# Optimization experiments

Measured on AMD Instinct MI355X. Metric: run time of the kernel, lower is better.

## Reference

```python
import jax, jax.numpy as jnp
import numpy as np

N_NODES = 100000
N_EDGES = 1600000
N_GRAPHS = 256
K_HOPS = 3


def setup_inputs() -> dict:
    key = jax.random.key(0)
    ks = jax.random.split(key, 10)
    x = jax.random.normal(ks[0], (N_NODES, 32), dtype=jnp.float32)
    edge_index = jax.random.randint(ks[1], (2, N_EDGES), 0, N_NODES, dtype=jnp.int32)
    batch = jnp.sort(jax.random.randint(ks[2], (N_NODES,), 0, N_GRAPHS, dtype=jnp.int32))
    gcn_w = jax.random.normal(ks[3], (64, 32), dtype=jnp.float32) * 0.1
    gcn_b = jax.random.normal(ks[4], (64,), dtype=jnp.float32) * 0.1
    w1 = jax.random.normal(ks[5], (32, 64), dtype=jnp.float32) * 0.1
    b1 = jax.random.normal(ks[6], (32,), dtype=jnp.float32) * 0.1
    w2 = jax.random.normal(ks[7], (16, 32), dtype=jnp.float32) * 0.1
    b2 = jax.random.normal(ks[8], (16,), dtype=jnp.float32) * 0.1
    return {"x": x, "edge_index": edge_index, "batch": batch,
            "gcn_w": gcn_w, "gcn_b": gcn_b, "w1": w1, "b1": b1, "w2": w2, "b2": b2}


def reference(x, edge_index, batch, gcn_w, gcn_b, w1, b1, w2, b2):
    N = x.shape[0]
    src, dst = edge_index[0], edge_index[1]
    # GCN symmetric normalization with self-loops: deg = in-degree + 1
    deg = jax.ops.segment_sum(jnp.ones_like(src, dtype=x.dtype), dst, num_segments=N) + 1.0
    norm = deg ** -0.5  # [N]
    h = x
    for _ in range(K_HOPS):
        # edge message: norm[src] * h[src], scattered to dst, scaled by norm[dst];
        # self-loop contributes norm[i]^2 * h[i]
        msg = h[src] * norm[src][:, None]                     # [E, C]
        agg = jax.ops.segment_sum(msg, dst, num_segments=N)    # [N, C]
        h = norm[:, None] * agg + (norm * norm)[:, None] * h
    h = jax.nn.relu(h @ gcn_w.T + gcn_b)                       # [N, hidden]
    # global mean pool per graph
    counts = jax.ops.segment_sum(jnp.ones((N,), x.dtype), batch, num_segments=N_GRAPHS)
    sums = jax.ops.segment_sum(h, batch, num_segments=N_GRAPHS)
    h_avg = sums / jnp.maximum(counts, 1.0)[:, None]           # [G, hidden]
    # classifier (dropout = identity in eval)
    h1 = jax.nn.relu(h_avg @ w1.T + b1)
    logits = h1 @ w2.T + b2                                    # [G, nc]
    return logits
```

## Files before the change

### kernel.cpp

```cpp
#include <hip/hip_runtime.h>

constexpr int NW    = 391;
constexpr int CH    = 8192;
constexpr int CAP_B = 8192;
constexpr int CAP_C = 10240;

__device__ __forceinline__ unsigned bf16_rne(float x) {
    unsigned u = __float_as_uint(x);
    u += 0x7fffu + ((u >> 16) & 1u);
    return u >> 16;
}
__device__ __forceinline__ unsigned pack2(float even, float odd) {
    return bf16_rne(even) | (bf16_rne(odd) << 16);
}
__device__ __forceinline__ float lo_f(unsigned u) { return __uint_as_float(u << 16); }
__device__ __forceinline__ float hi_f(unsigned u) { return __uint_as_float(u & 0xffff0000u); }


__global__ __launch_bounds__(512) void k_bucket(const int* __restrict__ src,
                                                const int* __restrict__ dst, int E,
                                                int* __restrict__ wcur, int* __restrict__ packed) {
    __shared__ int h[256];
    __shared__ int base[256];
    int t = threadIdx.x;
    if (t < 256) h[t] = 0;
    __syncthreads();
    int b0 = blockIdx.x * CH;
    int cnt = min(CH, E - b0);
    if (cnt == CH) {
        const int4* d4 = (const int4*)(dst + b0);
        for (int i = t; i < CH / 4; i += 512) {
            int4 v = d4[i];
            atomicAdd(&h[v.x / NW], 1); atomicAdd(&h[v.y / NW], 1);
            atomicAdd(&h[v.z / NW], 1); atomicAdd(&h[v.w / NW], 1);
        }
    } else {
        for (int i = t; i < cnt; i += 512) atomicAdd(&h[dst[b0 + i] / NW], 1);
    }
    __syncthreads();
    if (t < 256) { base[t] = atomicAdd(&wcur[t], h[t]); h[t] = 0; }
    __syncthreads();
    if (cnt == CH) {
        const int4* d4 = (const int4*)(dst + b0);
        const int4* s4 = (const int4*)(src + b0);
        for (int i = t; i < CH / 4; i += 512) {
            int4 dv = d4[i];
            int4 sv = s4[i];
            int da[4] = {dv.x, dv.y, dv.z, dv.w};
            int sa[4] = {sv.x, sv.y, sv.z, sv.w};
#pragma unroll
            for (int j = 0; j < 4; ++j) {
                int w = da[j] / NW;
                int l = da[j] - w * NW;
                int r = atomicAdd(&h[w], 1);
                int pos = base[w] + r;
                if (pos < CAP_B) packed[w * CAP_B + pos] = (l << 17) | sa[j];
            }
        }
    } else {
        for (int i = t; i < cnt; i += 512) {
            int d = dst[b0 + i];
            int s = src[b0 + i];
            int w = d / NW;
            int l = d - w * NW;
            int r = atomicAdd(&h[w], 1);
            int pos = base[w] + r;
            if (pos < CAP_B) packed[w * CAP_B + pos] = (l << 17) | s;
        }
    }
}


__global__ __launch_bounds__(512) void k_window(const int* __restrict__ packed,
                                                const int* __restrict__ wcur,
                                                float* __restrict__ norm,
                                                int2* __restrict__ rng,
                                                int* __restrict__ csr, int N, int W) {
    __shared__ int hist[NW];
    __shared__ int scan[512];
    __shared__ int cur[NW];
    int t = threadIdx.x, w = blockIdx.x;
    int lo = w * NW, nwn = min(NW, N - lo);
    for (int i = t; i < NW; i += 512) hist[i] = 0;
    __syncthreads();
    int cnt = min(wcur[w], CAP_B);
    const int* pk = packed + (size_t)w * CAP_B;
    for (int e = t; e < cnt; e += 512) atomicAdd(&hist[pk[e] >> 17], 1);
    __syncthreads();
    int d = (t < nwn) ? hist[t] : 0;
    if (t < nwn) norm[lo + t] = rsqrtf((float)(d + 1));
    int pd = (t < nwn) ? ((d + 7) & ~7) : 0;
    scan[t] = pd;
    __syncthreads();
    for (int s = 1; s < 512; s <<= 1) {
        int add = (t >= s) ? scan[t - s] : 0;
        __syncthreads();
        scan[t] += add;
        __syncthreads();
    }
    int base = w * CAP_C;
    int cend = base + scan[t];
    if (t < nwn) {
        rng[lo + t] = make_int2(cend - pd, cend);
        cur[t] = cend - pd;
    }
    if (w == W - 1 && t == 0) { norm[N] = 1.f; rng[N] = make_int2(0, 0); }
    __syncthreads();
    for (int e = t; e < cnt; e += 512) {
        int p = pk[e];
        int pos = atomicAdd(&cur[p >> 17], 1);
        csr[pos] = p & 0x1FFFF;
    }
    __syncthreads();
    if (t < nwn) {
        for (int pos = cur[t]; pos < cend; ++pos) csr[pos] = N;
    }
}


__global__ void k_prep(const float4* __restrict__ x, const float* __restrict__ norm,
                       uint2* __restrict__ outb, int N) {
    int t = blockIdx.x * blockDim.x + threadIdx.x;
    int i = t >> 3;
    if (i < N) {
        float n = norm[i];
        float4 v = x[t];
        outb[t] = make_uint2(pack2(v.x * n, v.y * n), pack2(v.z * n, v.w * n));
    } else if (i == N) {
        outb[t] = make_uint2(0u, 0u);
    }
}

template <bool LAST>
__global__ void k_hop(const uint2* __restrict__ tab, const float* __restrict__ norm,
                      const int2* __restrict__ rng, const int* __restrict__ csr,
                      uint2* __restrict__ outb, int N) {
    int group = (blockIdx.x * blockDim.x + threadIdx.x) >> 3;
    int l = threadIdx.x & 7;
    if (group > N) return;
    uint2 sv = tab[(size_t)group * 8 + l];
    float ax = lo_f(sv.x), ay = hi_f(sv.x), az = lo_f(sv.y), aw = hi_f(sv.y);
    int2 be = rng[group];
    int k = be.x;
    for (; k + 16 <= be.y; k += 16) {
        int e0 = csr[k + l];
        int e1 = csr[k + 8 + l];
        uint2 u[16];
#pragma unroll
        for (int j = 0; j < 8; ++j) {
            int s = __shfl(e0, j, 8);
            u[j] = tab[(size_t)s * 8 + l];
        }
#pragma unroll
        for (int j = 0; j < 8; ++j) {
            int s = __shfl(e1, j, 8);
            u[8 + j] = tab[(size_t)s * 8 + l];
        }
#pragma unroll
        for (int j = 0; j < 16; ++j) {
            ax += lo_f(u[j].x); ay += hi_f(u[j].x);
            az += lo_f(u[j].y); aw += hi_f(u[j].y);
        }
    }
    if (k < be.y) {
        int e = csr[k + l];
        uint2 u[8];
#pragma unroll
        for (int j = 0; j < 8; ++j) {
            int s = __shfl(e, j, 8);
            u[j] = tab[(size_t)s * 8 + l];
        }
#pragma unroll
        for (int j = 0; j < 8; ++j) {
            ax += lo_f(u[j].x); ay += hi_f(u[j].x);
            az += lo_f(u[j].y); aw += hi_f(u[j].y);
        }
    }
    float n = norm[group];
    float sc = LAST ? n : n * n;
    outb[(size_t)group * 8 + l] = make_uint2(pack2(ax * sc, ay * sc), pack2(az * sc, aw * sc));
}


__global__ __launch_bounds__(256) void k_feat(const uint2* __restrict__ hb,
                                              const float* __restrict__ gw,
                                              const float* __restrict__ gb,
                                              uint4* __restrict__ zb4, int N) {
    __shared__ float w[64 * 32];
    __shared__ float bs[64];
    int t = threadIdx.x;
    for (int i = t; i < 64 * 32; i += 256) w[i] = gw[i];
    if (t < 64) bs[t] = gb[t];
    __syncthreads();
    int n = blockIdx.x * 256 + t;
    if (n >= N) return;
    float hrow[32];
    const uint2* hr = hb + (size_t)n * 8;
#pragma unroll
    for (int q = 0; q < 8; ++q) {
        uint2 u = hr[q];
        hrow[q * 4] = lo_f(u.x); hrow[q * 4 + 1] = hi_f(u.x);
        hrow[q * 4 + 2] = lo_f(u.y); hrow[q * 4 + 3] = hi_f(u.y);
    }
#pragma unroll
    for (int c0 = 0; c0 < 64; c0 += 16) {
        float o[16];
#pragma unroll
        for (int cc = 0; cc < 16; ++cc) {
            const float* wr = &w[(c0 + cc) * 32];
            float d = bs[c0 + cc];
#pragma unroll
            for (int k = 0; k < 32; ++k) d += hrow[k] * wr[k];
            o[cc] = fmaxf(d, 0.f);
        }
        zb4[(size_t)n * 8 + (c0 >> 3)] =
            make_uint4(pack2(o[0], o[1]), pack2(o[2], o[3]), pack2(o[4], o[5]), pack2(o[6], o[7]));
        zb4[(size_t)n * 8 + (c0 >> 3) + 1] =
            make_uint4(pack2(o[8], o[9]), pack2(o[10], o[11]), pack2(o[12], o[13]), pack2(o[14], o[15]));
    }
}


__global__ __launch_bounds__(256) void k_pool(const uint2* __restrict__ zb2,
                                              const int* __restrict__ batch, int N,
                                              const float* __restrict__ w1, const float* __restrict__ b1,
                                              const float* __restrict__ w2, const float* __restrict__ b2,
                                              float* __restrict__ out) {
    __shared__ float4 part[16][17];
    __shared__ float havg[64];
    __shared__ float h1s[32];
    __shared__ int se[2];
    int t = threadIdx.x, g = blockIdx.x;
    if (t < 2) {
        int target = g + t;
        int lo = 0, hi = N;
        while (lo < hi) { int mid = (lo + hi) >> 1; if (batch[mid] < target) lo = mid + 1; else hi = mid; }
        se[t] = lo;
    }
    __syncthreads();
    int start = se[0], end = se[1];
    int q = t & 15;
    int r = t >> 4;
    float4 acc = make_float4(0.f, 0.f, 0.f, 0.f);
    for (int n = start + r; n < end; n += 16) {
        uint2 v = zb2[(size_t)n * 16 + q];
        acc.x += lo_f(v.x); acc.y += hi_f(v.x); acc.z += lo_f(v.y); acc.w += hi_f(v.y);
    }
    part[r][q] = acc;
    __syncthreads();
#pragma unroll
    for (int s = 8; s > 0; s >>= 1) {
        if (r < s) {
            float4 a = part[r][q], b = part[r + s][q];
            a.x += b.x; a.y += b.y; a.z += b.z; a.w += b.w;
            part[r][q] = a;
        }
        __syncthreads();
    }
    if (t < 16) {
        int cnt = end - start;
        float inv = 1.f / (float)(cnt > 0 ? cnt : 1);
        float4 a = part[0][t];
        havg[t * 4] = a.x * inv; havg[t * 4 + 1] = a.y * inv;
        havg[t * 4 + 2] = a.z * inv; havg[t * 4 + 3] = a.w * inv;
    }
    __syncthreads();
    if (t < 32) {
        float d = b1[t];
#pragma unroll
        for (int k = 0; k < 64; ++k) d += havg[k] * w1[t * 64 + k];
        h1s[t] = fmaxf(d, 0.f);
    }
    __syncthreads();
    if (t < 16) {
        float d = b2[t];
#pragma unroll
        for (int j = 0; j < 32; ++j) d += h1s[j] * w2[t * 32 + j];
        out[g * 16 + t] = d;
    }
}


extern "C" void kernel_launch(void* const* d_in, const int* in_sizes, int n_in,
                              void* d_out, int out_size, void* d_ws, size_t ws_size,
                              hipStream_t stream) {
    const float* x     = (const float*)d_in[0];
    const int*   ei    = (const int*)d_in[1];
    const int*   batch = (const int*)d_in[2];
    const float* gw    = (const float*)d_in[3];
    const float* gb    = (const float*)d_in[4];
    const float* w1    = (const float*)d_in[5];
    const float* b1    = (const float*)d_in[6];
    const float* w2    = (const float*)d_in[7];
    const float* b2    = (const float*)d_in[8];
    float* out = (float*)d_out;

    int N = in_sizes[2];
    int E = in_sizes[1] / 2;
    int G = out_size / 16;
    const int* srcp = ei;
    const int* dstp = ei + E;

    int W  = (N + NW - 1) / NW;
    int NB = (E + CH - 1) / CH;

    char* ws = (char*)d_ws;
    size_t off = 0;
    auto alloc = [&](size_t bytes) -> void* {
        void* p = ws + off;
        off += (bytes + 255) & ~(size_t)255;
        return p;
    };
    int*   wcur   = (int*)alloc(256 * 4);
    int*   packed = (int*)alloc((size_t)W * CAP_B * 4);
    int*   csr    = (int*)alloc((size_t)W * CAP_C * 4);
    int2*  rng    = (int2*)alloc((size_t)(N + 1) * 8);
    float* norm   = (float*)alloc((size_t)(N + 1) * 4);
    uint2* hbA    = (uint2*)alloc((size_t)(N + 1) * 64);
    uint2* hbB    = (uint2*)alloc((size_t)(N + 1) * 64);
    unsigned* zbuf = (unsigned*)alloc((size_t)N * 64 * 2);

    hipMemsetAsync(wcur, 0, 256 * 4, stream);

    int pb = ((N + 1) * 8 + 255) / 256;

    k_bucket<<<NB, 512, 0, stream>>>(srcp, dstp, E, wcur, packed);
    k_window<<<W, 512, 0, stream>>>(packed, wcur, norm, rng, csr, N, W);

    k_prep<<<pb, 256, 0, stream>>>((const float4*)x, norm, hbA, N);
    k_hop<false><<<pb, 256, 0, stream>>>(hbA, norm, rng, csr, hbB, N);
    k_hop<false><<<pb, 256, 0, stream>>>(hbB, norm, rng, csr, hbA, N);
    k_hop<true ><<<pb, 256, 0, stream>>>(hbA, norm, rng, csr, hbB, N);

    k_feat<<<(N + 255) / 256, 256, 0, stream>>>(hbB, gw, gb, (uint4*)zbuf, N);
    k_pool<<<G, 256, 0, stream>>>((const uint2*)zbuf, batch, N, w1, b1, w2, b2, out);
}
```

Before: 203.8 us.

## Fuse prep into window kernel, widen hop gathers to 16B, use wave-shuffle scan

The bf16 feature-table prep (norm-scaled x) moves into k_window, which already holds the window's norms in shared memory, so one launch and one norm reread go away. The block prefix scan switches from a barrier-heavy shared-memory loop to wavefront shuffle scans. k_hop now has 4 lanes per node, each gathering a uint4 (8 bf16), and reads the CSR 8 edges at a time through int2 loads, dropping the 16-edge unrolled path. Each gather is wider and fewer threads are launched, but fewer independent loads are in flight per node, which may reduce memory-level parallelism.

```diff
diff --git a/kernel.cpp b/kernel.cpp
--- a/kernel.cpp
+++ b/kernel.cpp
@@ -73,12 +73,16 @@
 
 __global__ __launch_bounds__(512) void k_window(const int* __restrict__ packed,
                                                 const int* __restrict__ wcur,
+                                                const float4* __restrict__ x4,
                                                 float* __restrict__ norm,
                                                 int2* __restrict__ rng,
-                                                int* __restrict__ csr, int N, int W) {
+                                                int* __restrict__ csr,
+                                                uint2* __restrict__ hb, int N, int W) {
     __shared__ int hist[NW];
-    __shared__ int scan[512];
+    __shared__ float snorm[NW];
+    __shared__ int pend[NW];
     __shared__ int cur[NW];
+    __shared__ int wpart[8];
     int t = threadIdx.x, w = blockIdx.x;
     int lo = w * NW, nwn = min(NW, N - lo);
     for (int i = t; i < NW; i += 512) hist[i] = 0;
@@ -88,20 +92,34 @@
     for (int e = t; e < cnt; e += 512) atomicAdd(&hist[pk[e] >> 17], 1);
     __syncthreads();
     int d = (t < nwn) ? hist[t] : 0;
-    if (t < nwn) norm[lo + t] = rsqrtf((float)(d + 1));
+    float nv = rsqrtf((float)(d + 1));
+    if (t < nwn) { snorm[t] = nv; norm[lo + t] = nv; }
     int pd = (t < nwn) ? ((d + 7) & ~7) : 0;
-    scan[t] = pd;
-    __syncthreads();
-    for (int s = 1; s < 512; s <<= 1) {
-        int add = (t >= s) ? scan[t - s] : 0;
-        __syncthreads();
-        scan[t] += add;
-        __syncthreads();
-    }
+    int lane = t & 63, wid = t >> 6;
+    int v = pd;
+#pragma unroll
+    for (int s = 1; s < 64; s <<= 1) {
+        int u = __shfl_up(v, s, 64);
+        if (lane >= s) v += u;
+    }
+    if (lane == 63) wpart[wid] = v;
+    __syncthreads();
+    if (t < 8) {
+        int z = wpart[t];
+#pragma unroll
+        for (int s = 1; s < 8; s <<= 1) {
+            int u = __shfl_up(z, s, 8);
+            if (t >= s) z += u;
+        }
+        wpart[t] = z;
+    }
+    __syncthreads();
+    int incl = v + (wid ? wpart[wid - 1] : 0);
     int base = w * CAP_C;
-    int cend = base + scan[t];
+    int cend = base + incl;
     if (t < nwn) {
         rng[lo + t] = make_int2(cend - pd, cend);
+        pend[t] = cend;
         cur[t] = cend - pd;
     }
     if (w == W - 1 && t == 0) { norm[N] = 1.f; rng[N] = make_int2(0, 0); }
@@ -113,72 +131,50 @@
     }
     __syncthreads();
     if (t < nwn) {
-        for (int pos = cur[t]; pos < cend; ++pos) csr[pos] = N;
-    }
-}
-
-
-__global__ void k_prep(const float4* __restrict__ x, const float* __restrict__ norm,
-                       uint2* __restrict__ outb, int N) {
-    int t = blockIdx.x * blockDim.x + threadIdx.x;
-    int i = t >> 3;
-    if (i < N) {
-        float n = norm[i];
-        float4 v = x[t];
-        outb[t] = make_uint2(pack2(v.x * n, v.y * n), pack2(v.z * n, v.w * n));
-    } else if (i == N) {
-        outb[t] = make_uint2(0u, 0u);
-    }
+        for (int pos = cur[t]; pos < pend[t]; ++pos) csr[pos] = N;
+    }
+    for (int idx = t; idx < nwn * 8; idx += 512) {
+        int node = idx >> 3, q = idx & 7;
+        float nn = snorm[node];
+        float4 vx = x4[(size_t)(lo + node) * 8 + q];
+        hb[(size_t)(lo + node) * 8 + q] =
+            make_uint2(pack2(vx.x * nn, vx.y * nn), pack2(vx.z * nn, vx.w * nn));
+    }
+    if (w == W - 1 && t < 8) hb[(size_t)N * 8 + t] = make_uint2(0u, 0u);
 }
 
 template <bool LAST>
-__global__ void k_hop(const uint2* __restrict__ tab, const float* __restrict__ norm,
-                      const int2* __restrict__ rng, const int* __restrict__ csr,
-                      uint2* __restrict__ outb, int N) {
-    int group = (blockIdx.x * blockDim.x + threadIdx.x) >> 3;
-    int l = threadIdx.x & 7;
+__global__ __launch_bounds__(256) void k_hop(const uint4* __restrict__ tab4,
+                                             const float* __restrict__ norm,
+                                             const int2* __restrict__ rng,
+                                             const int* __restrict__ csr,
+                                             uint4* __restrict__ out4, int N) {
+    int gid = blockIdx.x * blockDim.x + threadIdx.x;
+    int group = gid >> 2;
+    int l = threadIdx.x & 3;
     if (group > N) return;
-    uint2 sv = tab[(size_t)group * 8 + l];
-    float ax = lo_f(sv.x), ay = hi_f(sv.x), az = lo_f(sv.y), aw = hi_f(sv.y);
+    uint4 sv = tab4[(size_t)group * 4 + l];
+    float a0 = lo_f(sv.x), a1 = hi_f(sv.x), a2 = lo_f(sv.y), a3 = hi_f(sv.y);
+    float a4 = lo_f(sv.z), a5 = hi_f(sv.z), a6 = lo_f(sv.w), a7 = hi_f(sv.w);
     int2 be = rng[group];
-    int k = be.x;
-    for (; k + 16 <= be.y; k += 16) {
-        int e0 = csr[k + l];
-        int e1 = csr[k + 8 + l];
-        uint2 u[16];
+    for (int k = be.x; k < be.y; k += 8) {
+        int2 ev = *(const int2*)(csr + k + 2 * l);
+        uint4 u[8];
 #pragma unroll
         for (int j = 0; j < 8; ++j) {
-            int s = __shfl(e0, j, 8);
-            u[j] = tab[(size_t)s * 8 + l];
+            int s = __shfl((j & 1) ? ev.y : ev.x, j >> 1, 4);
+            u[j] = tab4[(size_t)s * 4 + l];
         }
 #pragma unroll
         for (int j = 0; j < 8; ++j) {
-            int s = __shfl(e1, j, 8);
-            u[8 + j] = tab[(size_t)s * 8 + l];
-        }
-#pragma unroll
-        for (int j = 0; j < 16; ++j) {
-            ax += lo_f(u[j].x); ay += hi_f(u[j].x);
-            az += lo_f(u[j].y); aw += hi_f(u[j].y);
-        }
-    }
-    if (k < be.y) {
-        int e = csr[k + l];
-        uint2 u[8];
-#pragma unroll
-        for (int j = 0; j < 8; ++j) {
-            int s = __shfl(e, j, 8);
-            u[j] = tab[(size_t)s * 8 + l];
-        }
-#pragma unroll
-        for (int j = 0; j < 8; ++j) {
-            ax += lo_f(u[j].x); ay += hi_f(u[j].x);
-            az += lo_f(u[j].y); aw += hi_f(u[j].y);
+            a0 += lo_f(u[j].x); a1 += hi_f(u[j].x); a2 += lo_f(u[j].y); a3 += hi_f(u[j].y);
+            a4 += lo_f(u[j].z); a5 += hi_f(u[j].z); a6 += lo_f(u[j].w); a7 += hi_f(u[j].w);
         }
     }
     float n = norm[group];
     float sc = LAST ? n : n * n;
-    outb[(size_t)group * 8 + l] = make_uint2(pack2(ax * sc, ay * sc), pack2(az * sc, aw * sc));
+    out4[(size_t)group * 4 + l] = make_uint4(pack2(a0 * sc, a1 * sc), pack2(a2 * sc, a3 * sc),
+                                             pack2(a4 * sc, a5 * sc), pack2(a6 * sc, a7 * sc));
 }
 
 
@@ -322,15 +318,14 @@
 
     hipMemsetAsync(wcur, 0, 256 * 4, stream);
 
-    int pb = ((N + 1) * 8 + 255) / 256;
+    int hb_blocks = ((N + 1) * 4 + 255) / 256;
 
     k_bucket<<<NB, 512, 0, stream>>>(srcp, dstp, E, wcur, packed);
-    k_window<<<W, 512, 0, stream>>>(packed, wcur, norm, rng, csr, N, W);
-
-    k_prep<<<pb, 256, 0, stream>>>((const float4*)x, norm, hbA, N);
-    k_hop<false><<<pb, 256, 0, stream>>>(hbA, norm, rng, csr, hbB, N);
-    k_hop<false><<<pb, 256, 0, stream>>>(hbB, norm, rng, csr, hbA, N);
-    k_hop<true ><<<pb, 256, 0, stream>>>(hbA, norm, rng, csr, hbB, N);
+    k_window<<<W, 512, 0, stream>>>(packed, wcur, (const float4*)x, norm, rng, csr, hbA, N, W);
+
+    k_hop<false><<<hb_blocks, 256, 0, stream>>>((const uint4*)hbA, norm, rng, csr, (uint4*)hbB, N);
+    k_hop<false><<<hb_blocks, 256, 0, stream>>>((const uint4*)hbB, norm, rng, csr, (uint4*)hbA, N);
+    k_hop<true ><<<hb_blocks, 256, 0, stream>>>((const uint4*)hbA, norm, rng, csr, (uint4*)hbB, N);
 
     k_feat<<<(N + 255) / 256, 256, 0, stream>>>(hbB, gw, gb, (uint4*)zbuf, N);
     k_pool<<<G, 256, 0, stream>>>((const uint2*)zbuf, batch, N, w1, b1, w2, b2, out);
```

After: 211.5 us. 3.8% more time.

## Split each hop into two source-half passes and fuse prep into window kernel

Applied to the files above, without the earlier changes.

Each node's CSR neighbour list is split into two segments by source index (below or above N/2), and each hop runs as two passes. Each pass gathers from only half of the feature table, which should fit the working set better in cache, and the partial sum goes through a bf16 buffer. The x-scaling prep kernel is folded into the window kernel, and its Hillis-Steele shared scan is replaced by a wavefront shuffle scan. The cost is twice as many hop launches, an extra round-trip of the partial buffer, more padding in the CSR, and an extra bf16 rounding of the intermediate sum.

```diff
diff --git a/kernel.cpp b/kernel.cpp
--- a/kernel.cpp
+++ b/kernel.cpp
@@ -3,7 +3,7 @@
 constexpr int NW    = 391;
 constexpr int CH    = 8192;
 constexpr int CAP_B = 8192;
-constexpr int CAP_C = 10240;
+constexpr int CAP_C = 12288;
 
 __device__ __forceinline__ unsigned bf16_rne(float x) {
     unsigned u = __float_as_uint(x);
@@ -73,76 +73,103 @@
 
 __global__ __launch_bounds__(512) void k_window(const int* __restrict__ packed,
                                                 const int* __restrict__ wcur,
+                                                const float4* __restrict__ x4,
                                                 float* __restrict__ norm,
-                                                int2* __restrict__ rng,
-                                                int* __restrict__ csr, int N, int W) {
-    __shared__ int hist[NW];
-    __shared__ int scan[512];
-    __shared__ int cur[NW];
+                                                int4* __restrict__ rng4,
+                                                int* __restrict__ csr,
+                                                uint2* __restrict__ hb, int N, int W, int HALF) {
+    __shared__ int hist2[NW * 2];
+    __shared__ float snorm[NW];
+    __shared__ int begl[NW];
+    __shared__ int cur2[NW * 2];
+    __shared__ int wpart[8];
     int t = threadIdx.x, w = blockIdx.x;
     int lo = w * NW, nwn = min(NW, N - lo);
-    for (int i = t; i < NW; i += 512) hist[i] = 0;
+    for (int i = t; i < NW * 2; i += 512) hist2[i] = 0;
     __syncthreads();
     int cnt = min(wcur[w], CAP_B);
     const int* pk = packed + (size_t)w * CAP_B;
-    for (int e = t; e < cnt; e += 512) atomicAdd(&hist[pk[e] >> 17], 1);
-    __syncthreads();
-    int d = (t < nwn) ? hist[t] : 0;
-    if (t < nwn) norm[lo + t] = rsqrtf((float)(d + 1));
-    int pd = (t < nwn) ? ((d + 7) & ~7) : 0;
-    scan[t] = pd;
-    __syncthreads();
-    for (int s = 1; s < 512; s <<= 1) {
-        int add = (t >= s) ? scan[t - s] : 0;
-        __syncthreads();
-        scan[t] += add;
-        __syncthreads();
-    }
-    int base = w * CAP_C;
-    int cend = base + scan[t];
-    if (t < nwn) {
-        rng[lo + t] = make_int2(cend - pd, cend);
-        cur[t] = cend - pd;
-    }
-    if (w == W - 1 && t == 0) { norm[N] = 1.f; rng[N] = make_int2(0, 0); }
-    __syncthreads();
     for (int e = t; e < cnt; e += 512) {
         int p = pk[e];
-        int pos = atomicAdd(&cur[p >> 17], 1);
-        csr[pos] = p & 0x1FFFF;
-    }
-    __syncthreads();
+        atomicAdd(&hist2[(p >> 17) * 2 + ((p & 0x1FFFF) >= HALF)], 1);
+    }
+    __syncthreads();
+    int dA = 0, dB = 0;
+    if (t < nwn) { dA = hist2[t * 2]; dB = hist2[t * 2 + 1]; }
+    float nv = rsqrtf((float)(dA + dB + 1));
+    if (t < nwn) { snorm[t] = nv; norm[lo + t] = nv; }
+    int pdA = (t < nwn) ? ((dA + 7) & ~7) : 0;
+    int pdB = (t < nwn) ? ((dB + 7) & ~7) : 0;
+    int pd = pdA + pdB;
+    int lane = t & 63, wid = t >> 6;
+    int v = pd;
+#pragma unroll
+    for (int s = 1; s < 64; s <<= 1) {
+        int u = __shfl_up(v, s, 64);
+        if (lane >= s) v += u;
+    }
+    if (lane == 63) wpart[wid] = v;
+    __syncthreads();
+    if (t < 8) {
+        int z = wpart[t];
+#pragma unroll
+        for (int s = 1; s < 8; s <<= 1) {
+            int u = __shfl_up(z, s, 8);
+            if (t >= s) z += u;
+        }
+        wpart[t] = z;
+    }
+    __syncthreads();
+    int incl = v + (wid ? wpart[wid - 1] : 0);
+    int beg = w * CAP_C + incl - pd;
     if (t < nwn) {
-        for (int pos = cur[t]; pos < cend; ++pos) csr[pos] = N;
-    }
-}
-
-
-__global__ void k_prep(const float4* __restrict__ x, const float* __restrict__ norm,
-                       uint2* __restrict__ outb, int N) {
-    int t = blockIdx.x * blockDim.x + threadIdx.x;
-    int i = t >> 3;
-    if (i < N) {
-        float n = norm[i];
-        float4 v = x[t];
-        outb[t] = make_uint2(pack2(v.x * n, v.y * n), pack2(v.z * n, v.w * n));
-    } else if (i == N) {
-        outb[t] = make_uint2(0u, 0u);
-    }
-}
-
-template <bool LAST>
+        begl[t] = beg;
+        rng4[lo + t] = make_int4(beg, beg + pdA, beg + pdA + pdB, 0);
+        cur2[t * 2] = beg;
+        cur2[t * 2 + 1] = beg + pdA;
+    }
+    if (w == W - 1 && t == 0) { norm[N] = 1.f; rng4[N] = make_int4(0, 0, 0, 0); }
+    __syncthreads();
+    for (int e = t; e < cnt; e += 512) {
+        int p = pk[e];
+        int s = p & 0x1FFFF;
+        int pos = atomicAdd(&cur2[(p >> 17) * 2 + (s >= HALF)], 1);
+        csr[pos] = s;
+    }
+    __syncthreads();
+    if (t < nwn) {
+        int b = begl[t];
+        int dA2 = hist2[t * 2], dB2 = hist2[t * 2 + 1];
+        int pA = (dA2 + 7) & ~7, pB = (dB2 + 7) & ~7;
+        for (int pos = b + dA2; pos < b + pA; ++pos) csr[pos] = N;
+        int mb = b + pA;
+        for (int pos = mb + dB2; pos < mb + pB; ++pos) csr[pos] = N;
+    }
+    for (int idx = t; idx < nwn * 8; idx += 512) {
+        int node = idx >> 3, q = idx & 7;
+        float nn = snorm[node];
+        float4 vx = x4[(size_t)(lo + node) * 8 + q];
+        hb[(size_t)(lo + node) * 8 + q] =
+            make_uint2(pack2(vx.x * nn, vx.y * nn), pack2(vx.z * nn, vx.w * nn));
+    }
+    if (w == W - 1 && t < 8) hb[(size_t)N * 8 + t] = make_uint2(0u, 0u);
+}
+
+template <int PASS, bool LAST>
 __global__ void k_hop(const uint2* __restrict__ tab, const float* __restrict__ norm,
-                      const int2* __restrict__ rng, const int* __restrict__ csr,
-                      uint2* __restrict__ outb, int N) {
+                      const int4* __restrict__ rng4, const int* __restrict__ csr,
+                      const uint2* __restrict__ pin, uint2* __restrict__ outb, int N) {
     int group = (blockIdx.x * blockDim.x + threadIdx.x) >> 3;
     int l = threadIdx.x & 7;
     if (group > N) return;
-    uint2 sv = tab[(size_t)group * 8 + l];
+    uint2 sv = (PASS == 0) ? tab[(size_t)group * 8 + l]
+                           : pin[(size_t)group * 8 + l];
     float ax = lo_f(sv.x), ay = hi_f(sv.x), az = lo_f(sv.y), aw = hi_f(sv.y);
-    int2 be = rng[group];
-    int k = be.x;
-    for (; k + 16 <= be.y; k += 16) {
+    int4 r = rng4[group];
+    int kb = (PASS == 0) ? r.x : r.y;
+    int ke = (PASS == 0) ? r.y : r.z;
+    int k = kb;
+    for (; k + 16 <= ke; k += 16) {
         int e0 = csr[k + l];
         int e1 = csr[k + 8 + l];
         uint2 u[16];
@@ -162,7 +189,7 @@
             az += lo_f(u[j].y); aw += hi_f(u[j].y);
         }
     }
-    if (k < be.y) {
+    if (k < ke) {
         int e = csr[k + l];
         uint2 u[8];
 #pragma unroll
@@ -176,9 +203,14 @@
             az += lo_f(u[j].y); aw += hi_f(u[j].y);
         }
     }
-    float n = norm[group];
-    float sc = LAST ? n : n * n;
-    outb[(size_t)group * 8 + l] = make_uint2(pack2(ax * sc, ay * sc), pack2(az * sc, aw * sc));
+    if (PASS == 0) {
+        outb[(size_t)group * 8 + l] = make_uint2(pack2(ax, ay), pack2(az, aw));
+    } else {
+        float n = norm[group];
+        float sc = LAST ? n : n * n;
+        outb[(size_t)group * 8 + l] =
+            make_uint2(pack2(ax * sc, ay * sc), pack2(az * sc, aw * sc));
+    }
 }
 
 
@@ -301,8 +333,9 @@
     const int* srcp = ei;
     const int* dstp = ei + E;
 
-    int W  = (N + NW - 1) / NW;
-    int NB = (E + CH - 1) / CH;
+    int W    = (N + NW - 1) / NW;
+    int NB   = (E + CH - 1) / CH;
+    int HALF = N / 2;
 
     char* ws = (char*)d_ws;
     size_t off = 0;
@@ -314,10 +347,11 @@
     int*   wcur   = (int*)alloc(256 * 4);
     int*   packed = (int*)alloc((size_t)W * CAP_B * 4);
     int*   csr    = (int*)alloc((size_t)W * CAP_C * 4);
-    int2*  rng    = (int2*)alloc((size_t)(N + 1) * 8);
+    int4*  rng4   = (int4*)alloc((size_t)(N + 1) * 16);
     float* norm   = (float*)alloc((size_t)(N + 1) * 4);
     uint2* hbA    = (uint2*)alloc((size_t)(N + 1) * 64);
     uint2* hbB    = (uint2*)alloc((size_t)(N + 1) * 64);
+    uint2* partb  = (uint2*)alloc((size_t)(N + 1) * 64);
     unsigned* zbuf = (unsigned*)alloc((size_t)N * 64 * 2);
 
     hipMemsetAsync(wcur, 0, 256 * 4, stream);
@@ -325,12 +359,14 @@
     int pb = ((N + 1) * 8 + 255) / 256;
 
     k_bucket<<<NB, 512, 0, stream>>>(srcp, dstp, E, wcur, packed);
-    k_window<<<W, 512, 0, stream>>>(packed, wcur, norm, rng, csr, N, W);
-
-    k_prep<<<pb, 256, 0, stream>>>((const float4*)x, norm, hbA, N);
-    k_hop<false><<<pb, 256, 0, stream>>>(hbA, norm, rng, csr, hbB, N);
-    k_hop<false><<<pb, 256, 0, stream>>>(hbB, norm, rng, csr, hbA, N);
-    k_hop<true ><<<pb, 256, 0, stream>>>(hbA, norm, rng, csr, hbB, N);
+    k_window<<<W, 512, 0, stream>>>(packed, wcur, (const float4*)x, norm, rng4, csr, hbA, N, W, HALF);
+
+    k_hop<0, false><<<pb, 256, 0, stream>>>(hbA, norm, rng4, csr, nullptr, partb, N);
+    k_hop<1, false><<<pb, 256, 0, stream>>>(hbA, norm, rng4, csr, partb, hbB, N);
+    k_hop<0, false><<<pb, 256, 0, stream>>>(hbB, norm, rng4, csr, nullptr, partb, N);
+    k_hop<1, false><<<pb, 256, 0, stream>>>(hbB, norm, rng4, csr, partb, hbA, N);
+    k_hop<0, false><<<pb, 256, 0, stream>>>(hbA, norm, rng4, csr, nullptr, partb, N);
+    k_hop<1, true ><<<pb, 256, 0, stream>>>(hbA, norm, rng4, csr, partb, hbB, N);
 
     k_feat<<<(N + 255) / 256, 256, 0, stream>>>(hbB, gw, gb, (uint4*)zbuf, N);
     k_pool<<<G, 256, 0, stream>>>((const uint2*)zbuf, batch, N, w1, b1, w2, b2, out);
```

Measured after the change: 224.1 us. 1.1x slower.
